# Performance work log

Hardware: AMD Instinct MI355X
Metric: run time of the kernel (lower is better)

## Reference

```python
import jax, jax.numpy as jnp
import numpy as np

B_, L_, DIN, DM, DS, DR, K = 2, 1024, 1024, 2048, 16, 128, 4


def setup_inputs() -> dict:
    key = jax.random.key(0)
    ks = jax.random.split(key, 10)
    s = lambda k, shape, sc=0.02: (jax.random.normal(k, shape, jnp.float32) * sc)
    A_init = jnp.tile(jnp.arange(1, DS + 1, dtype=jnp.float32)[None, :], (DM, 1))  # (DM, DS)
    return {
        'x_in': jax.random.normal(ks[0], (B_, L_, DIN), jnp.float32),
        'W_in': s(ks[1], (DIN, DM)),
        'W_res': s(ks[2], (DIN, DM)),
        'W_out': s(ks[3], (DM, DIN)),
        'conv_w': s(ks[4], (DM, K), 0.1),   # depthwise conv weight (torch shape (DM,1,K) squeezed)
        'conv_b': jnp.zeros((DM,), jnp.float32),
        'A_log': jnp.log(A_init),
        'D': jnp.ones((DM,), jnp.float32),
        'W_B': s(ks[5], (DM, DS)),
        'W_C': s(ks[6], (DM, DS)),
        'W_dt': s(ks[7], (DM, DR)),
        'dt_w': s(ks[8], (DR, DM)),
        'dt_b': jnp.zeros((DM,), jnp.float32),
    }


def reference(x_in, W_in, W_res, W_out, conv_w, conv_b, A_log, D, W_B, W_C, W_dt, dt_w, dt_b):
    Bb, L, _ = x_in.shape
    x = x_in @ W_in                     # (B, L, DM)
    res = x_in @ W_res                  # (B, L, DM)
    # Causal depthwise conv1d: pad left k-1, truncate to L (matches Conv1d(padding=k-1)[:, :, :L])
    xp = jnp.pad(x, ((0, 0), (K - 1, 0), (0, 0)))
    xc = conv_b
    for i in range(K):
        xc = xc + xp[:, i:i + L, :] * conv_w[:, i]
    xc = jax.nn.silu(xc)                # (B, L, DM)
    # Selective SSM (fused_ssm)
    A = -jnp.exp(A_log)                 # (DM, DS)
    Bp = xc @ W_B                       # (B, L, DS)
    Cp = xc @ W_C                       # (B, L, DS)
    delta = jax.nn.softplus((xc @ W_dt) @ dt_w + dt_b)  # (B, L, DM)
    dA = jnp.exp(delta[..., None] * A)                       # (B, L, DM, DS)
    dBu = delta[..., None] * Bp[:, :, None, :] * xc[..., None]  # (B, L, DM, DS)

    def step(h, inp):
        dA_t, dBu_t, C_t = inp
        h = dA_t * h + dBu_t                         # (B, DM, DS)
        y = jnp.einsum('bdn,bn->bd', h, C_t)         # (B, DM)
        return h, y

    h0 = jnp.zeros((Bb, DM, DS), jnp.float32)
    _, ys = jax.lax.scan(step, h0, (dA.transpose(1, 0, 2, 3), dBu.transpose(1, 0, 2, 3), Cp.transpose(1, 0, 2)))
    y = ys.transpose(1, 0, 2) + D * xc  # (B, L, DM)
    y = y * jax.nn.silu(res)
    return y @ W_out                    # (B, L, DIN)
```

## Files before the change

### kernel.cpp

```cpp
#include <hip/hip_runtime.h>
#include <hip/hip_bf16.h>

constexpr int B_  = 2;
constexpr int L_  = 1024;
constexpr int DIN = 1024;
constexpr int DM  = 2048;
constexpr int DS  = 16;
constexpr int DR  = 128;
constexpr int KC  = 4;
constexpr int M_  = B_ * L_;
constexpr int NP2 = 256;
constexpr int NPC = 160;
constexpr int KSLICES = 8;
constexpr int KSL = DM / KSLICES;

constexpr int NC = 32;
constexpr int CL = L_ / NC;
constexpr int S_ = B_ * DM * DS;

typedef __bf16 bf16x8 __attribute__((ext_vector_type(8)));
typedef float  f32x4  __attribute__((ext_vector_type(4)));

__device__ __forceinline__ void gload_lds16(const void* g, void* l) {
    __builtin_amdgcn_global_load_lds(
        (const __attribute__((address_space(1))) void*)g,
        (__attribute__((address_space(3))) void*)l, 16, 0, 0);
}

__device__ __forceinline__ void transpose_block(const float* __restrict__ in,
                                                __bf16* __restrict__ out,
                                                int R, int C, int bx, int by, int t) {
    __shared__ float tile[32][33];
    int tx = t & 31, ty = t >> 5;
    #pragma unroll
    for (int j = 0; j < 32; j += 8)
        tile[ty + j][tx] = in[(size_t)(by * 32 + ty + j) * C + (bx * 32 + tx)];
    __syncthreads();
    #pragma unroll
    for (int j = 0; j < 32; j += 8)
        out[(size_t)(bx * 32 + ty + j) * R + (by * 32 + tx)] = (__bf16)tile[tx][ty + j];
}

__global__ void prep_all(const float* __restrict__ x_in, const float* __restrict__ W_in,
                         const float* __restrict__ W_res, const float* __restrict__ W_out,
                         const float* __restrict__ dt_w,
                         const float* __restrict__ W_B, const float* __restrict__ W_C,
                         const float* __restrict__ W_dt, const float* __restrict__ conv_w,
                         __bf16* __restrict__ xinB, __bf16* __restrict__ WinT,
                         __bf16* __restrict__ WresT, __bf16* __restrict__ WoutT,
                         __bf16* __restrict__ dtwT, __bf16* __restrict__ projW,
                         float* __restrict__ cwT) {
    int blk = blockIdx.x, t = threadIdx.x;
    if (blk < 8192) {
        int i = blk * 256 + t;
        xinB[i] = (__bf16)x_in[i];
    } else if (blk < 10240) {
        int b = blk - 8192;
        transpose_block(W_in, WinT, DIN, DM, b % 64, b / 64, t);
    } else if (blk < 12288) {
        int b = blk - 10240;
        transpose_block(W_res, WresT, DIN, DM, b % 64, b / 64, t);
    } else if (blk < 14336) {
        int b = blk - 12288;
        transpose_block(W_out, WoutT, DM, DIN, b % 32, b / 32, t);
    } else if (blk < 14592) {
        int b = blk - 14336;
        transpose_block(dt_w, dtwT, DR, DM, b % 64, b / 64, t);
    } else if (blk < 16640) {
        int i = (blk - 14592) * 256 + t;
        int k = i % DM;
        int n = i / DM;
        float v = 0.f;
        if (n < 16)        v = W_B[(size_t)k * DS + n];
        else if (n < 32)   v = W_C[(size_t)k * DS + (n - 16)];
        else if (n < 160)  v = W_dt[(size_t)k * DR + (n - 32)];
        projW[i] = (__bf16)v;
    } else {
        int j = (blk - 16640) * 256 + t;
        int tap = j / DM, d = j % DM;
        cwT[j] = conv_w[d * KC + tap];
    }
}

__global__ void reduce_split(const __bf16* __restrict__ PpartB, float* __restrict__ Bp,
                             float* __restrict__ Cp, __bf16* __restrict__ dtmpB) {
    int i = blockIdx.x * 256 + threadIdx.x;
    int row = i / NPC, c = i % NPC;
    float v = 0.f;
    #pragma unroll
    for (int ks = 0; ks < KSLICES; ks++)
        v += (float)PpartB[(size_t)ks * M_ * NPC + i];
    if (c < 16)       Bp[(size_t)row * DS + c] = v;
    else if (c < 32)  Cp[(size_t)row * DS + (c - 16)] = v;
    else              dtmpB[(size_t)row * DR + (c - 32)] = (__bf16)v;
}

template<int EPI>
__global__ void gemm_tile128(const __bf16* __restrict__ A, const __bf16* __restrict__ BT,
                             float* __restrict__ Cf, __bf16* __restrict__ Cb,
                             const float* __restrict__ bias, int M, int N, int K,
                             int lda, int ldb) {
    __shared__ __bf16 sA[128 * 32];
    __shared__ __bf16 sB[128 * 32];
    int t = threadIdx.x;
    int lane = t & 63, w = t >> 6;
    int wm = w >> 1, wn = w & 1;
    int m0 = blockIdx.y * 128, n0 = blockIdx.x * 128;
    int kbase = blockIdx.z * K;
    int q = lane >> 4, rr = lane & 15;

    f32x4 acc[4][4] = {};

    int srow = t >> 2;
    int slot = t & 3;

    for (int kt = 0; kt < K; kt += 32) {
        __syncthreads();
        #pragma unroll
        for (int rnd = 0; rnd < 2; rnd++) {
            int row = srow + rnd * 64;
            int gkb = slot ^ ((row >> 1) & 3);
            const __bf16* ga = A  + (size_t)(m0 + row) * lda + kbase + kt + gkb * 8;
            const __bf16* gb = BT + (size_t)(n0 + row) * ldb + kbase + kt + gkb * 8;
            __bf16* la = sA + rnd * 2048 + w * 512;
            __bf16* lb = sB + rnd * 2048 + w * 512;
            gload_lds16(ga, la);
            gload_lds16(gb, lb);
        }
        __syncthreads();

        bf16x8 af[4], bfr[4];
        #pragma unroll
        for (int i = 0; i < 4; i++) {
            int rowA = wm * 64 + i * 16 + rr;
            af[i] = *(const bf16x8*)(sA + rowA * 32 + ((q ^ ((rowA >> 1) & 3)) * 8));
            int rowB = wn * 64 + i * 16 + rr;
            bfr[i] = *(const bf16x8*)(sB + rowB * 32 + ((q ^ ((rowB >> 1) & 3)) * 8));
        }
        #pragma unroll
        for (int i = 0; i < 4; i++)
            #pragma unroll
            for (int j = 0; j < 4; j++)
                acc[i][j] = __builtin_amdgcn_mfma_f32_16x16x32_bf16(af[i], bfr[j], acc[i][j], 0, 0, 0);
    }

    #pragma unroll
    for (int i = 0; i < 4; i++) {
        #pragma unroll
        for (int j = 0; j < 4; j++) {
            int col = n0 + wn * 64 + j * 16 + rr;
            #pragma unroll
            for (int jj = 0; jj < 4; jj++) {
                int row = m0 + wm * 64 + i * 16 + q * 4 + jj;
                float v = acc[i][j][jj];
                if (EPI == 1) {
                    float z = v + bias[col];
                    Cb[(size_t)row * N + col] = (__bf16)((z > 20.f) ? z : log1pf(__expf(z)));
                } else if (EPI == 2) {
                    if (col < DM) ((__bf16*)Cf)[(size_t)row * DM + col] = (__bf16)v;
                    else          Cb[(size_t)row * DM + (col - DM)] = (__bf16)v;
                } else {
                    if (col < NPC)
                        Cb[(size_t)blockIdx.z * M * NPC + (size_t)row * NPC + col] = (__bf16)v;
                }
            }
        }
    }
}

__global__ void gemm_out64(const __bf16* __restrict__ A, const __bf16* __restrict__ BT,
                           float* __restrict__ C, int M, int N, int K, int lda, int ldb) {
    __shared__ __bf16 sA[128 * 32];
    __shared__ __bf16 sB[64 * 32];
    int t = threadIdx.x;
    int lane = t & 63, w = t >> 6;
    int m0 = blockIdx.y * 128, n0 = blockIdx.x * 64;
    int q = lane >> 4, rr = lane & 15;

    f32x4 acc[2][4] = {};
    int srow = t >> 2;
    int slot = t & 3;

    for (int kt = 0; kt < K; kt += 32) {
        __syncthreads();
        #pragma unroll
        for (int rnd = 0; rnd < 2; rnd++) {
            int row = srow + rnd * 64;
            int gkb = slot ^ ((row >> 1) & 3);
            const __bf16* ga = A + (size_t)(m0 + row) * lda + kt + gkb * 8;
            __bf16* la = sA + rnd * 2048 + w * 512;
            gload_lds16(ga, la);
        }
        {
            int row = srow;
            int gkb = slot ^ ((row >> 1) & 3);
            const __bf16* gb = BT + (size_t)(n0 + row) * ldb + kt + gkb * 8;
            __bf16* lb = sB + w * 512;
            gload_lds16(gb, lb);
        }
        __syncthreads();

        bf16x8 af[2], bfr[4];
        #pragma unroll
        for (int i = 0; i < 2; i++) {
            int rowA = w * 32 + i * 16 + rr;
            af[i] = *(const bf16x8*)(sA + rowA * 32 + ((q ^ ((rowA >> 1) & 3)) * 8));
        }
        #pragma unroll
        for (int j = 0; j < 4; j++) {
            int rowB = j * 16 + rr;
            bfr[j] = *(const bf16x8*)(sB + rowB * 32 + ((q ^ ((rowB >> 1) & 3)) * 8));
        }
        #pragma unroll
        for (int i = 0; i < 2; i++)
            #pragma unroll
            for (int j = 0; j < 4; j++)
                acc[i][j] = __builtin_amdgcn_mfma_f32_16x16x32_bf16(af[i], bfr[j], acc[i][j], 0, 0, 0);
    }

    #pragma unroll
    for (int i = 0; i < 2; i++) {
        #pragma unroll
        for (int j = 0; j < 4; j++) {
            int col = n0 + j * 16 + rr;
            #pragma unroll
            for (int jj = 0; jj < 4; jj++) {
                int row = m0 + w * 32 + i * 16 + q * 4 + jj;
                C[(size_t)row * N + col] = acc[i][j][jj];
            }
        }
    }
}

__global__ void conv_silu(const __bf16* __restrict__ x, const float* __restrict__ cwT,
                          const float* __restrict__ bias, __bf16* __restrict__ xcB) {
    int row = blockIdx.x;
    int d   = threadIdx.x * 8;
    int l   = row % L_;
    size_t base = (size_t)row * DM + d;

    float acc[8];
    {
        const f32x4* b4 = (const f32x4*)(bias + d);
        f32x4 b0 = b4[0], b1 = b4[1];
        #pragma unroll
        for (int q = 0; q < 4; q++) { acc[q] = b0[q]; acc[4 + q] = b1[q]; }
    }
    #pragma unroll
    for (int i = 0; i < KC; i++) {
        int li = l - (KC - 1) + i;
        if (li >= 0) {
            bf16x8 xv = *(const bf16x8*)(x + base + (size_t)(i - (KC - 1)) * DM);
            const f32x4* w4 = (const f32x4*)(cwT + (size_t)i * DM + d);
            f32x4 w0 = w4[0], w1 = w4[1];
            #pragma unroll
            for (int q = 0; q < 4; q++) {
                acc[q]     = fmaf((float)xv[q],     w0[q], acc[q]);
                acc[4 + q] = fmaf((float)xv[4 + q], w1[q], acc[4 + q]);
            }
        }
    }
    bf16x8 out;
    #pragma unroll
    for (int q = 0; q < 8; q++) {
        float v = acc[q] / (1.f + __expf(-acc[q]));
        out[q] = (__bf16)v;
    }
    *(bf16x8*)(xcB + base) = out;
}

__global__ void scan_phase1(const __bf16* __restrict__ delta, const __bf16* __restrict__ xc,
                            const float* __restrict__ Bp, const float* __restrict__ A_log,
                            __bf16* __restrict__ aprodB, __bf16* __restrict__ cendB) {
    int blk = blockIdx.x;
    int c   = blk % NC;
    int rem = blk / NC;
    int dmt = rem % (DM / 256);
    int b   = rem / (DM / 256);
    int t   = threadIdx.x;
    int dm  = dmt * 256 + t;
    int l0  = c * CL;

    __shared__ float sB[CL * DS];
    sB[t]       = Bp[((size_t)b * L_ + l0) * DS + t];
    sB[t + 256] = Bp[((size_t)b * L_ + l0) * DS + t + 256];
    __syncthreads();

    float Aval[DS];
    {
        const f32x4* Ap = (const f32x4*)(A_log + (size_t)dm * DS);
        #pragma unroll
        for (int r4 = 0; r4 < 4; r4++) {
            f32x4 a = Ap[r4];
            #pragma unroll
            for (int q = 0; q < 4; q++) Aval[r4 * 4 + q] = -__expf(a[q]);
        }
    }

    float h[DS], ap[DS];
    #pragma unroll
    for (int i = 0; i < DS; i++) { h[i] = 0.f; ap[i] = 1.f; }

    size_t base = ((size_t)b * L_ + l0) * DM + dm;
    #pragma unroll 4
    for (int j = 0; j < CL; j++) {
        float dl  = (float)delta[base + (size_t)j * DM];
        float xv  = (float)xc[base + (size_t)j * DM];
        float cmn = dl * xv;
        const f32x4* sB4 = (const f32x4*)(sB + j * DS);
        #pragma unroll
        for (int r4 = 0; r4 < 4; r4++) {
            f32x4 bv = sB4[r4];
            #pragma unroll
            for (int q = 0; q < 4; q++) {
                int i = r4 * 4 + q;
                float dA = __expf(dl * Aval[i]);
                ap[i] *= dA;
                h[i] = fmaf(dA, h[i], cmn * bv[q]);
            }
        }
    }

    size_t s = ((size_t)(b * DM + dm)) * DS;
    #pragma unroll
    for (int r8 = 0; r8 < 2; r8++) {
        bf16x8 va, vh;
        #pragma unroll
        for (int q = 0; q < 8; q++) { va[q] = (__bf16)ap[r8 * 8 + q]; vh[q] = (__bf16)h[r8 * 8 + q]; }
        ((bf16x8*)(aprodB + (size_t)c * S_ + s))[r8] = va;
        ((bf16x8*)(cendB  + (size_t)c * S_ + s))[r8] = vh;
    }
}

__global__ void scan_phase2(const __bf16* __restrict__ aprodB, const __bf16* __restrict__ cendB,
                            __bf16* __restrict__ hinitB) {
    int u8 = (blockIdx.x * 256 + threadIdx.x) * 8;
    float h[8];
    #pragma unroll
    for (int q = 0; q < 8; q++) h[q] = 0.f;
    #pragma unroll
    for (int c = 0; c < NC; c++) {
        bf16x8 a  = *(const bf16x8*)(aprodB + (size_t)c * S_ + u8);
        bf16x8 ce = *(const bf16x8*)(cendB  + (size_t)c * S_ + u8);
        bf16x8 ho;
        #pragma unroll
        for (int q = 0; q < 8; q++) {
            ho[q] = (__bf16)h[q];
            h[q] = fmaf((float)a[q], h[q], (float)ce[q]);
        }
        *(bf16x8*)(hinitB + (size_t)c * S_ + u8) = ho;
    }
}

__global__ void scan_phase3(const __bf16* __restrict__ delta, const __bf16* __restrict__ xc,
                            const float* __restrict__ Bp, const float* __restrict__ Cp,
                            const __bf16* __restrict__ res, const float* __restrict__ A_log,
                            const float* __restrict__ Dw, const __bf16* __restrict__ hinitB,
                            __bf16* __restrict__ ybar) {
    int blk = blockIdx.x;
    int c   = blk % NC;
    int rem = blk / NC;
    int dmt = rem % (DM / 256);
    int b   = rem / (DM / 256);
    int t   = threadIdx.x;
    int dm  = dmt * 256 + t;
    int l0  = c * CL;

    __shared__ float sB[CL * DS];
    __shared__ float sC[CL * DS];
    sB[t]       = Bp[((size_t)b * L_ + l0) * DS + t];
    sB[t + 256] = Bp[((size_t)b * L_ + l0) * DS + t + 256];
    sC[t]       = Cp[((size_t)b * L_ + l0) * DS + t];
    sC[t + 256] = Cp[((size_t)b * L_ + l0) * DS + t + 256];
    __syncthreads();

    float Aval[DS];
    {
        const f32x4* Ap = (const f32x4*)(A_log + (size_t)dm * DS);
        #pragma unroll
        for (int r4 = 0; r4 < 4; r4++) {
            f32x4 a = Ap[r4];
            #pragma unroll
            for (int q = 0; q < 4; q++) Aval[r4 * 4 + q] = -__expf(a[q]);
        }
    }
    float Dval = Dw[dm];

    float h[DS];
    {
        size_t s = ((size_t)(b * DM + dm)) * DS;
        #pragma unroll
        for (int r8 = 0; r8 < 2; r8++) {
            bf16x8 v = ((const bf16x8*)(hinitB + (size_t)c * S_ + s))[r8];
            #pragma unroll
            for (int q = 0; q < 8; q++) h[r8 * 8 + q] = (float)v[q];
        }
    }

    size_t base = ((size_t)b * L_ + l0) * DM + dm;
    #pragma unroll 4
    for (int j = 0; j < CL; j++) {
        float dl  = (float)delta[base + (size_t)j * DM];
        float xv  = (float)xc[base + (size_t)j * DM];
        float rv  = (float)res[base + (size_t)j * DM];
        float cmn = dl * xv;
        float y = 0.f;
        const f32x4* sB4 = (const f32x4*)(sB + j * DS);
        const f32x4* sC4 = (const f32x4*)(sC + j * DS);
        #pragma unroll
        for (int r4 = 0; r4 < 4; r4++) {
            f32x4 bv = sB4[r4];
            f32x4 cv = sC4[r4];
            #pragma unroll
            for (int q = 0; q < 4; q++) {
                int i = r4 * 4 + q;
                float dA = __expf(dl * Aval[i]);
                h[i] = fmaf(dA, h[i], cmn * bv[q]);
                y = fmaf(h[i], cv[q], y);
            }
        }
        float g = rv / (1.f + __expf(-rv));
        ybar[base + (size_t)j * DM] = (__bf16)((y + Dval * xv) * g);
    }
}

extern "C" void kernel_launch(void* const* d_in, const int* in_sizes, int n_in,
                              void* d_out, int out_size, void* d_ws, size_t ws_size,
                              hipStream_t stream) {
    const float* x_in   = (const float*)d_in[0];
    const float* W_in   = (const float*)d_in[1];
    const float* W_res  = (const float*)d_in[2];
    const float* W_out  = (const float*)d_in[3];
    const float* conv_w = (const float*)d_in[4];
    const float* conv_b = (const float*)d_in[5];
    const float* A_log  = (const float*)d_in[6];
    const float* Dw     = (const float*)d_in[7];
    const float* W_B    = (const float*)d_in[8];
    const float* W_C    = (const float*)d_in[9];
    const float* W_dt   = (const float*)d_in[10];
    const float* dt_w   = (const float*)d_in[11];
    const float* dt_b   = (const float*)d_in[12];

    float* ws_f = (float*)d_ws;
    float* Bp    = ws_f;
    float* Cp    = Bp + (size_t)M_ * DS;
    float* cwT   = Cp + (size_t)M_ * DS;
    __bf16* bf_base = (__bf16*)(cwT + (size_t)KC * DM);
    __bf16* ybar   = bf_base;
    __bf16* xinB   = ybar   + (size_t)M_ * DM;
    __bf16* WinT   = xinB   + (size_t)M_ * DIN;
    __bf16* WresT  = WinT   + (size_t)DM * DIN;
    __bf16* WoutT  = WresT  + (size_t)DM * DIN;
    __bf16* xB     = WoutT  + (size_t)DIN * DM;
    __bf16* xcB    = xB     + (size_t)M_ * DM;
    __bf16* projW  = xcB    + (size_t)M_ * DM;
    __bf16* dtwT   = projW  + (size_t)NP2 * DM;
    __bf16* dtmpB  = dtwT   + (size_t)DM * DR;
    __bf16* deltaB = dtmpB  + (size_t)M_ * DR;
    __bf16* resB   = deltaB + (size_t)M_ * DM;
    __bf16* aprodB = resB   + (size_t)M_ * DM;
    __bf16* cendB  = aprodB + (size_t)NC * S_;
    __bf16* hinitB = cendB  + (size_t)NC * S_;
    __bf16* PpartB = hinitB + (size_t)NC * S_;

    prep_all<<<16672, 256, 0, stream>>>(x_in, W_in, W_res, W_out, dt_w, W_B, W_C, W_dt,
                                        conv_w, xinB, WinT, WresT, WoutT, dtwT, projW, cwT);

    gemm_tile128<2><<<dim3((2 * DM) / 128, M_ / 128, 1), 256, 0, stream>>>(
        xinB, WinT, (float*)xB, resB, nullptr, M_, 2 * DM, DIN, DIN, DIN);

    conv_silu<<<M_, 256, 0, stream>>>(xB, cwT, conv_b, xcB);

    gemm_tile128<4><<<dim3(NP2 / 128, M_ / 128, KSLICES), 256, 0, stream>>>(
        xcB, projW, nullptr, PpartB, nullptr, M_, NP2, KSL, DM, DM);
    reduce_split<<<(M_ * NPC) / 256, 256, 0, stream>>>(PpartB, Bp, Cp, dtmpB);

    gemm_tile128<1><<<dim3(DM / 128, M_ / 128, 1), 256, 0, stream>>>(
        dtmpB, dtwT, nullptr, deltaB, dt_b, M_, DM, DR, DR, DR);

    int nblk = B_ * (DM / 256) * NC;
    scan_phase1<<<nblk, 256, 0, stream>>>(deltaB, xcB, Bp, A_log, aprodB, cendB);
    scan_phase2<<<S_ / (256 * 8), 256, 0, stream>>>(aprodB, cendB, hinitB);
    scan_phase3<<<nblk, 256, 0, stream>>>(deltaB, xcB, Bp, Cp, resB, A_log, Dw, hinitB, ybar);

    gemm_out64<<<dim3(DIN / 64, M_ / 128), 256, 0, stream>>>(
        ybar, WoutT, (float*)d_out, M_, DIN, DM, DM, DM);
}
```

Before: 267.0 us.

## Double-buffer LDS tiles in GEMM kernels and widen scan_phase2 parallelism

Both GEMM kernels get two LDS buffers, so the global-to-LDS load for the next K tile is issued before the MFMAs on the current tile, with one barrier per iteration instead of two. The goal is to hide global load latency behind compute. LDS use doubles, which can lower occupancy. Separately, scan_phase2 moves from 8 state elements per thread to 1, launching 8x more threads to raise parallelism on the sequential chunk scan, at the cost of scalar rather than 16-byte loads.

```diff
diff --git a/kernel.cpp b/kernel.cpp
--- a/kernel.cpp
+++ b/kernel.cpp
@@ -100,8 +100,8 @@
                              float* __restrict__ Cf, __bf16* __restrict__ Cb,
                              const float* __restrict__ bias, int M, int N, int K,
                              int lda, int ldb) {
-    __shared__ __bf16 sA[128 * 32];
-    __shared__ __bf16 sB[128 * 32];
+    __shared__ __bf16 sA[2][128 * 32];
+    __shared__ __bf16 sB[2][128 * 32];
     int t = threadIdx.x;
     int lane = t & 63, w = t >> 6;
     int wm = w >> 1, wn = w & 1;
@@ -114,34 +114,50 @@
     int srow = t >> 2;
     int slot = t & 3;
 
-    for (int kt = 0; kt < K; kt += 32) {
-        __syncthreads();
-        #pragma unroll
-        for (int rnd = 0; rnd < 2; rnd++) {
-            int row = srow + rnd * 64;
-            int gkb = slot ^ ((row >> 1) & 3);
-            const __bf16* ga = A  + (size_t)(m0 + row) * lda + kbase + kt + gkb * 8;
-            const __bf16* gb = BT + (size_t)(n0 + row) * ldb + kbase + kt + gkb * 8;
-            __bf16* la = sA + rnd * 2048 + w * 512;
-            __bf16* lb = sB + rnd * 2048 + w * 512;
-            gload_lds16(ga, la);
-            gload_lds16(gb, lb);
-        }
-        __syncthreads();
+    const int nt = K >> 5;
+
+    #pragma unroll
+    for (int rnd = 0; rnd < 2; rnd++) {
+        int row = srow + rnd * 64;
+        int gkb = slot ^ ((row >> 1) & 3);
+        gload_lds16(A  + (size_t)(m0 + row) * lda + kbase + gkb * 8,
+                    &sA[0][rnd * 2048 + w * 512]);
+        gload_lds16(BT + (size_t)(n0 + row) * ldb + kbase + gkb * 8,
+                    &sB[0][rnd * 2048 + w * 512]);
+    }
+    __syncthreads();
+
+    int cur = 0;
+    for (int tix = 0; tix < nt; tix++) {
+        if (tix + 1 < nt) {
+            int kt = (tix + 1) << 5;
+            #pragma unroll
+            for (int rnd = 0; rnd < 2; rnd++) {
+                int row = srow + rnd * 64;
+                int gkb = slot ^ ((row >> 1) & 3);
+                gload_lds16(A  + (size_t)(m0 + row) * lda + kbase + kt + gkb * 8,
+                            &sA[cur ^ 1][rnd * 2048 + w * 512]);
+                gload_lds16(BT + (size_t)(n0 + row) * ldb + kbase + kt + gkb * 8,
+                            &sB[cur ^ 1][rnd * 2048 + w * 512]);
+            }
+        }
 
         bf16x8 af[4], bfr[4];
         #pragma unroll
         for (int i = 0; i < 4; i++) {
             int rowA = wm * 64 + i * 16 + rr;
-            af[i] = *(const bf16x8*)(sA + rowA * 32 + ((q ^ ((rowA >> 1) & 3)) * 8));
+            af[i] = *(const bf16x8*)(&sA[cur][rowA * 32 + ((q ^ ((rowA >> 1) & 3)) * 8)]);
             int rowB = wn * 64 + i * 16 + rr;
-            bfr[i] = *(const bf16x8*)(sB + rowB * 32 + ((q ^ ((rowB >> 1) & 3)) * 8));
+            bfr[i] = *(const bf16x8*)(&sB[cur][rowB * 32 + ((q ^ ((rowB >> 1) & 3)) * 8)]);
         }
         #pragma unroll
         for (int i = 0; i < 4; i++)
             #pragma unroll
             for (int j = 0; j < 4; j++)
                 acc[i][j] = __builtin_amdgcn_mfma_f32_16x16x32_bf16(af[i], bfr[j], acc[i][j], 0, 0, 0);
+
+        __syncthreads();
+        cur ^= 1;
     }
 
     #pragma unroll
@@ -170,8 +186,8 @@
 
 __global__ void gemm_out64(const __bf16* __restrict__ A, const __bf16* __restrict__ BT,
                            float* __restrict__ C, int M, int N, int K, int lda, int ldb) {
-    __shared__ __bf16 sA[128 * 32];
-    __shared__ __bf16 sB[64 * 32];
+    __shared__ __bf16 sA[2][128 * 32];
+    __shared__ __bf16 sB[2][64 * 32];
     int t = threadIdx.x;
     int lane = t & 63, w = t >> 6;
     int m0 = blockIdx.y * 128, n0 = blockIdx.x * 64;
@@ -181,41 +197,57 @@
     int srow = t >> 2;
     int slot = t & 3;
 
-    for (int kt = 0; kt < K; kt += 32) {
-        __syncthreads();
+    const int nt = K >> 5;
+
+    {
         #pragma unroll
         for (int rnd = 0; rnd < 2; rnd++) {
             int row = srow + rnd * 64;
             int gkb = slot ^ ((row >> 1) & 3);
-            const __bf16* ga = A + (size_t)(m0 + row) * lda + kt + gkb * 8;
-            __bf16* la = sA + rnd * 2048 + w * 512;
-            gload_lds16(ga, la);
-        }
-        {
-            int row = srow;
-            int gkb = slot ^ ((row >> 1) & 3);
-            const __bf16* gb = BT + (size_t)(n0 + row) * ldb + kt + gkb * 8;
-            __bf16* lb = sB + w * 512;
-            gload_lds16(gb, lb);
-        }
-        __syncthreads();
+            gload_lds16(A + (size_t)(m0 + row) * lda + gkb * 8,
+                        &sA[0][rnd * 2048 + w * 512]);
+        }
+        int gkb = slot ^ ((srow >> 1) & 3);
+        gload_lds16(BT + (size_t)(n0 + srow) * ldb + gkb * 8,
+                    &sB[0][w * 512]);
+    }
+    __syncthreads();
+
+    int cur = 0;
+    for (int tix = 0; tix < nt; tix++) {
+        if (tix + 1 < nt) {
+            int kt = (tix + 1) << 5;
+            #pragma unroll
+            for (int rnd = 0; rnd < 2; rnd++) {
+                int row = srow + rnd * 64;
+                int gkb = slot ^ ((row >> 1) & 3);
+                gload_lds16(A + (size_t)(m0 + row) * lda + kt + gkb * 8,
+                            &sA[cur ^ 1][rnd * 2048 + w * 512]);
+            }
+            int gkb = slot ^ ((srow >> 1) & 3);
+            gload_lds16(BT + (size_t)(n0 + srow) * ldb + kt + gkb * 8,
+                        &sB[cur ^ 1][w * 512]);
+        }
 
         bf16x8 af[2], bfr[4];
         #pragma unroll
         for (int i = 0; i < 2; i++) {
             int rowA = w * 32 + i * 16 + rr;
-            af[i] = *(const bf16x8*)(sA + rowA * 32 + ((q ^ ((rowA >> 1) & 3)) * 8));
+            af[i] = *(const bf16x8*)(&sA[cur][rowA * 32 + ((q ^ ((rowA >> 1) & 3)) * 8)]);
         }
         #pragma unroll
         for (int j = 0; j < 4; j++) {
             int rowB = j * 16 + rr;
-            bfr[j] = *(const bf16x8*)(sB + rowB * 32 + ((q ^ ((rowB >> 1) & 3)) * 8));
+            bfr[j] = *(const bf16x8*)(&sB[cur][rowB * 32 + ((q ^ ((rowB >> 1) & 3)) * 8)]);
         }
         #pragma unroll
         for (int i = 0; i < 2; i++)
             #pragma unroll
             for (int j = 0; j < 4; j++)
                 acc[i][j] = __builtin_amdgcn_mfma_f32_16x16x32_bf16(af[i], bfr[j], acc[i][j], 0, 0, 0);
+
+        __syncthreads();
+        cur ^= 1;
     }
 
     #pragma unroll
@@ -334,21 +366,14 @@
 
 __global__ void scan_phase2(const __bf16* __restrict__ aprodB, const __bf16* __restrict__ cendB,
                             __bf16* __restrict__ hinitB) {
-    int u8 = (blockIdx.x * 256 + threadIdx.x) * 8;
-    float h[8];
-    #pragma unroll
-    for (int q = 0; q < 8; q++) h[q] = 0.f;
+    int u = blockIdx.x * 256 + threadIdx.x;
+    float h = 0.f;
     #pragma unroll
     for (int c = 0; c < NC; c++) {
-        bf16x8 a  = *(const bf16x8*)(aprodB + (size_t)c * S_ + u8);
-        bf16x8 ce = *(const bf16x8*)(cendB  + (size_t)c * S_ + u8);
-        bf16x8 ho;
-        #pragma unroll
-        for (int q = 0; q < 8; q++) {
-            ho[q] = (__bf16)h[q];
-            h[q] = fmaf((float)a[q], h[q], (float)ce[q]);
-        }
-        *(bf16x8*)(hinitB + (size_t)c * S_ + u8) = ho;
+        float a  = (float)aprodB[(size_t)c * S_ + u];
+        float ce = (float)cendB [(size_t)c * S_ + u];
+        hinitB[(size_t)c * S_ + u] = (__bf16)h;
+        h = fmaf(a, h, ce);
     }
 }
 
@@ -480,7 +505,7 @@
 
     int nblk = B_ * (DM / 256) * NC;
     scan_phase1<<<nblk, 256, 0, stream>>>(deltaB, xcB, Bp, A_log, aprodB, cendB);
-    scan_phase2<<<S_ / (256 * 8), 256, 0, stream>>>(aprodB, cendB, hinitB);
+    scan_phase2<<<S_ / 256, 256, 0, stream>>>(aprodB, cendB, hinitB);
     scan_phase3<<<nblk, 256, 0, stream>>>(deltaB, xcB, Bp, Cp, resB, A_log, Dw, hinitB, ybar);
 
     gemm_out64<<<dim3(DIN / 64, M_ / 128), 256, 0, stream>>>(
```

Measured after the change: 263.3 us. No clear change (-1.4%).
